# Optimization experiments

Measured on AMD Instinct MI355X. Metric: run time of the kernel, lower is better.

The kernel has to match this reference:

```python
import jax, jax.numpy as jnp
import numpy as np

B, T, E, H = 4, 4096, 1024, 16
D = E // H          # per-head hidden_size in fla LinearAttention (num_heads=1)
CH = 64             # fused-chunk chunk size


def setup_inputs() -> dict:
    key = jax.random.key(0)
    k1, k2, k3, k4, k5 = jax.random.split(key, 5)
    s = 1.0 / np.sqrt(D).astype(np.float32)
    x = jax.random.normal(k1, (B, T, E), dtype=jnp.float32)
    Wq = jax.random.normal(k2, (D, D), dtype=jnp.float32) * s
    Wk = jax.random.normal(k3, (D, D), dtype=jnp.float32) * s
    Wv = jax.random.normal(k4, (D, D), dtype=jnp.float32) * s
    Wo = jax.random.normal(k5, (D, D), dtype=jnp.float32) * s
    return {"x": x, "Wq": Wq, "Wk": Wk, "Wv": Wv, "Wo": Wo}


def _phi(x):
    # fla 'elu' feature map: elu(x) + 1 (positive features)
    return jax.nn.elu(x) + 1.0


def _linear_attn_fused_chunk(q, k, v):
    # q,k,v: [B,H,T,D]; causal linear attention via chunked recurrence.
    b, h, t, d = q.shape
    n = t // CH
    # [N, B, H, CH, D] so scan runs over chunks
    qc = q.reshape(b, h, n, CH, d).transpose(2, 0, 1, 3, 4)
    kc = k.reshape(b, h, n, CH, d).transpose(2, 0, 1, 3, 4)
    vc = v.reshape(b, h, n, CH, d).transpose(2, 0, 1, 3, 4)
    mask = jnp.tril(jnp.ones((CH, CH), dtype=q.dtype))  # causal, diag inclusive

    def step(S, inp):
        qi, ki, vi = inp                                   # [B,H,CH,D]
        attn = jnp.einsum('bhck,bhek->bhce', qi, ki) * mask  # intra-chunk scores
        o_intra = jnp.einsum('bhce,bhed->bhcd', attn, vi)
        o_inter = jnp.einsum('bhck,bhkd->bhcd', qi, S)       # past-state term
        S_new = S + jnp.einsum('bhck,bhcd->bhkd', ki, vi)    # state update
        return S_new, o_intra + o_inter

    S0 = jnp.zeros((b, h, d, d), dtype=q.dtype)
    _, oc = jax.lax.scan(step, S0, (qc, kc, vc))           # oc: [N,B,H,CH,D]
    return oc.transpose(1, 2, 0, 3, 4).reshape(b, h, t, d)


def reference(x, Wq, Wk, Wv, Wo):
    # split outer heads: [B,T,E] -> [B,H,T,D]
    xh = x.reshape(B, T, H, D).transpose(0, 2, 1, 3)
    # shared [D,D] projections (fla LinearAttention with num_heads=1), tied elu feature map on q,k
    q = _phi(jnp.einsum('bhtd,de->bhte', xh, Wq))
    k = _phi(jnp.einsum('bhtd,de->bhte', xh, Wk))
    v = jnp.einsum('bhtd,de->bhte', xh, Wv)
    o = _linear_attn_fused_chunk(q, k, v)                  # no feature-map norm, identity output norm
    o = jnp.einsum('bhtd,de->bhte', o, Wo)
    return o.transpose(0, 2, 1, 3).reshape(B, T, E)
```

## Files before the change

kernel.cpp:

```cpp
#include <hip/hip_runtime.h>
#include <cstdint>
#include <cstddef>

constexpr int Bc = 4, Tc = 4096, Ec = 1024, Hc = 16, Dc = 64, CHc = 64;
constexpr int NSEG = 16;
constexpr int SEGT = Tc / NSEG;
constexpr int NCHUNK = SEGT / CHc;
constexpr int LP = 72;

typedef __attribute__((ext_vector_type(8))) short short8;
typedef __attribute__((ext_vector_type(4))) short short4v;
typedef __attribute__((ext_vector_type(4))) float f32x4;

__device__ __forceinline__ unsigned short f2bf(float f) {
  union { float f; unsigned int u; } v; v.f = f;
  return (unsigned short)((v.u + 0x7FFFu + ((v.u >> 16) & 1u)) >> 16);
}
__device__ __forceinline__ float bf2f(unsigned short u) {
  union { unsigned int u; float f; } v; v.u = ((unsigned int)u) << 16;
  return v.f;
}
__device__ __forceinline__ float phi_elu1(float x) {
  return x > 0.f ? x + 1.f : __expf(x);
}
__device__ __forceinline__ short8 ld8(const unsigned short* p) {
  return *reinterpret_cast<const short8*>(p);
}
__device__ __forceinline__ void st8(unsigned short* p, short8 v) {
  *reinterpret_cast<short8*>(p) = v;
}

#define MFMA_B16(a, b, c) __builtin_amdgcn_mfma_f32_16x16x32_bf16((a), (b), (c), 0, 0, 0)

__device__ __forceinline__ void cvt_store16(unsigned short* dst, float4 f0, float4 f1,
                                            float4 f2, float4 f3) {
  union { unsigned short us[16]; short8 v[2]; } pk;
  pk.us[0] = f2bf(f0.x);  pk.us[1] = f2bf(f0.y);  pk.us[2] = f2bf(f0.z);  pk.us[3] = f2bf(f0.w);
  pk.us[4] = f2bf(f1.x);  pk.us[5] = f2bf(f1.y);  pk.us[6] = f2bf(f1.z);  pk.us[7] = f2bf(f1.w);
  pk.us[8] = f2bf(f2.x);  pk.us[9] = f2bf(f2.y);  pk.us[10] = f2bf(f2.z); pk.us[11] = f2bf(f2.w);
  pk.us[12] = f2bf(f3.x); pk.us[13] = f2bf(f3.y); pk.us[14] = f2bf(f3.z); pk.us[15] = f2bf(f3.w);
  st8(dst, pk.v[0]); st8(dst + 8, pk.v[1]);
}

__global__ void prep_weights(const float* __restrict__ Wq, const float* __restrict__ Wk,
                             const float* __restrict__ Wv, const float* __restrict__ Wo,
                             unsigned short* __restrict__ wT) {
  int tid = blockIdx.x * blockDim.x + threadIdx.x;
  if (tid >= 4 * Dc * Dc) return;
  int m = tid >> 12, i = tid & 4095, d = i >> 6, e = i & 63;
  const float* W = (m == 0) ? Wq : (m == 1) ? Wk : (m == 2) ? Wv : Wo;
  wT[m * 4096 + e * 64 + d] = f2bf(W[d * 64 + e]);
}

__global__ __launch_bounds__(256, 3) void pass1_kvseg(
    const float* __restrict__ x, const unsigned short* __restrict__ wT,
    float* __restrict__ kvseg) {
  __shared__ unsigned short s_x[2 * 64 * LP];
  __shared__ unsigned short s_kT[64 * LP];
  __shared__ unsigned short s_vT[64 * LP];

  const int tid = threadIdx.x;
  const int w = tid >> 6, lane = tid & 63, lr = lane & 15, lq = lane >> 4;
  const int bh = blockIdx.x, sg = blockIdx.y;
  const int b = bh >> 4, h = bh & 15;
  const float* xbase = x + ((size_t)b * Tc + (size_t)sg * SEGT) * Ec + h * Dc;
  const unsigned short* wkT = wT + 4096;
  const unsigned short* wvT = wT + 2 * 4096;
  const int sr = tid >> 2, sc = tid & 3;
  const f32x4 zero4 = {0.f, 0.f, 0.f, 0.f};

  short8 awk[2], awv[2];
#pragma unroll
  for (int kk = 0; kk < 2; ++kk) {
    awk[kk] = ld8(wkT + (w * 16 + lr) * 64 + kk * 32 + lq * 8);
    awv[kk] = ld8(wvT + (w * 16 + lr) * 64 + kk * 32 + lq * 8);
  }

  {
    const float4* xf = reinterpret_cast<const float4*>(xbase + (size_t)sr * Ec + sc * 16);
    cvt_store16(&s_x[sr * LP + sc * 16], xf[0], xf[1], xf[2], xf[3]);
  }
  __syncthreads();

  f32x4 sacc[4] = {zero4, zero4, zero4, zero4};

#pragma unroll
  for (int ci = 0; ci < NCHUNK; ++ci) {
    unsigned short* sxc = &s_x[(ci & 1) * 64 * LP];
    unsigned short* sxn = &s_x[(1 - (ci & 1)) * 64 * LP];

    float4 pf0, pf1, pf2, pf3;
    if (ci < NCHUNK - 1) {
      const float4* xf = reinterpret_cast<const float4*>(
          xbase + (size_t)((ci + 1) * CHc + sr) * Ec + sc * 16);
      pf0 = xf[0]; pf1 = xf[1]; pf2 = xf[2]; pf3 = xf[3];
    }

    f32x4 ak[4] = {zero4, zero4, zero4, zero4};
    f32x4 av[4] = {zero4, zero4, zero4, zero4};
#pragma unroll
    for (int c = 0; c < 4; ++c) {
#pragma unroll
      for (int kk = 0; kk < 2; ++kk) {
        short8 bx = ld8(&sxc[(c * 16 + lr) * LP + kk * 32 + lq * 8]);
        ak[c] = MFMA_B16(awk[kk], bx, ak[c]);
        av[c] = MFMA_B16(awv[kk], bx, av[c]);
      }
    }
#pragma unroll
    for (int c = 0; c < 4; ++c) {
#pragma unroll
      for (int j = 0; j < 4; ++j) {
        int r = w * 16 + lq * 4 + j;
        s_kT[r * LP + c * 16 + lr] = f2bf(phi_elu1(ak[c][j]));
        s_vT[r * LP + c * 16 + lr] = f2bf(av[c][j]);
      }
    }
    __syncthreads();

    short8 avt[2];
#pragma unroll
    for (int kk = 0; kk < 2; ++kk)
      avt[kk] = ld8(&s_vT[(w * 16 + lr) * LP + kk * 32 + lq * 8]);
#pragma unroll
    for (int c = 0; c < 4; ++c)
#pragma unroll
      for (int kk = 0; kk < 2; ++kk)
        sacc[c] = MFMA_B16(avt[kk], ld8(&s_kT[(c * 16 + lr) * LP + kk * 32 + lq * 8]), sacc[c]);

    if (ci < NCHUNK - 1)
      cvt_store16(&sxn[sr * LP + sc * 16], pf0, pf1, pf2, pf3);
    __syncthreads();
  }

  float* dst = kvseg + ((size_t)(bh * NSEG + sg)) * 4096;
#pragma unroll
  for (int c = 0; c < 4; ++c)
#pragma unroll
    for (int j = 0; j < 4; ++j)
      dst[(w * 16 + lq * 4 + j) * 64 + c * 16 + lr] = sacc[c][j];
}

__global__ __launch_bounds__(256) void pass2_prefix(const float* __restrict__ kvseg,
                                                    unsigned short* __restrict__ sprefix) {
  const int bh = blockIdx.x, tile = blockIdx.y;
  const int e = tile * 1024 + threadIdx.x * 4;
  const float* src = kvseg + (size_t)bh * NSEG * 4096 + e;
  unsigned short* dst = sprefix + (size_t)bh * NSEG * 4096 + e;
  float4 vals[NSEG];
#pragma unroll
  for (int s = 0; s < NSEG; ++s)
    vals[s] = *reinterpret_cast<const float4*>(src + (size_t)s * 4096);
  float a0 = 0.f, a1 = 0.f, a2 = 0.f, a3 = 0.f;
#pragma unroll
  for (int s = 0; s < NSEG; ++s) {
    short4v sv;
    sv[0] = (short)f2bf(a0); sv[1] = (short)f2bf(a1);
    sv[2] = (short)f2bf(a2); sv[3] = (short)f2bf(a3);
    *reinterpret_cast<short4v*>(dst + (size_t)s * 4096) = sv;
    a0 += vals[s].x; a1 += vals[s].y; a2 += vals[s].z; a3 += vals[s].w;
  }
}

__global__ __launch_bounds__(256, 2) void pass3_main(
    const float* __restrict__ x, const unsigned short* __restrict__ wT,
    const unsigned short* __restrict__ sprefix, float* __restrict__ out) {
  __shared__ unsigned short s_x[2 * 64 * LP];
  __shared__ unsigned short s_q [64 * LP];
  __shared__ unsigned short s_k [64 * LP];
  __shared__ unsigned short s_kT[64 * LP];
  __shared__ unsigned short s_vT[64 * LP];
  __shared__ unsigned short s_Sb[64 * LP];

  const int tid = threadIdx.x;
  const int w = tid >> 6, lane = tid & 63, lr = lane & 15, lq = lane >> 4;
  const int bh = blockIdx.x, sg = blockIdx.y;
  const int b = bh >> 4, h = bh & 15;
  const float* xbase = x + ((size_t)b * Tc + (size_t)sg * SEGT) * Ec + h * Dc;
  float* obase = out + ((size_t)b * Tc + (size_t)sg * SEGT) * Ec + h * Dc;
  const unsigned short* wqT = wT;
  const unsigned short* wkT = wT + 4096;
  const unsigned short* wvT = wT + 2 * 4096;
  const unsigned short* woT = wT + 3 * 4096;
  const unsigned short* Sg = sprefix + ((size_t)(bh * NSEG + sg)) * 4096;
  const int sr = tid >> 2, sc = tid & 3;
  const int arow = (w * 16 + lr) * LP;
  const f32x4 zero4 = {0.f, 0.f, 0.f, 0.f};

  short8 bwq[4][2], bwk[4][2], bwo[4][2], awv[2];
#pragma unroll
  for (int c = 0; c < 4; ++c) {
#pragma unroll
    for (int kk = 0; kk < 2; ++kk) {
      bwq[c][kk] = ld8(wqT + (c * 16 + lr) * 64 + kk * 32 + lq * 8);
      bwk[c][kk] = ld8(wkT + (c * 16 + lr) * 64 + kk * 32 + lq * 8);
      bwo[c][kk] = ld8(woT + (c * 16 + lr) * 64 + kk * 32 + lq * 8);
    }
  }
#pragma unroll
  for (int kk = 0; kk < 2; ++kk)
    awv[kk] = ld8(wvT + (w * 16 + lr) * 64 + kk * 32 + lq * 8);

  {
    const float4* xf = reinterpret_cast<const float4*>(xbase + (size_t)sr * Ec + sc * 16);
    cvt_store16(&s_x[sr * LP + sc * 16], xf[0], xf[1], xf[2], xf[3]);
    const unsigned short* sp = Sg + sr * 64 + (tid & 3) * 16;
    st8(&s_Sb[sr * LP + (tid & 3) * 16], ld8(sp));
    st8(&s_Sb[sr * LP + (tid & 3) * 16 + 8], ld8(sp + 8));
  }
  __syncthreads();

  f32x4 sacc[4];
#pragma unroll
  for (int c = 0; c < 4; ++c)
#pragma unroll
    for (int j = 0; j < 4; ++j)
      sacc[c][j] = bf2f(s_Sb[(w * 16 + lq * 4 + j) * LP + c * 16 + lr]);

#pragma unroll
  for (int ci = 0; ci < NCHUNK; ++ci) {
    unsigned short* sxc = &s_x[(ci & 1) * 64 * LP];
    unsigned short* sxn = &s_x[(1 - (ci & 1)) * 64 * LP];

    float4 pf0, pf1, pf2, pf3;
    if (ci < NCHUNK - 1) {
      const float4* xf = reinterpret_cast<const float4*>(
          xbase + (size_t)((ci + 1) * CHc + sr) * Ec + sc * 16);
      pf0 = xf[0]; pf1 = xf[1]; pf2 = xf[2]; pf3 = xf[3];
    }

    short8 ax[2];
    ax[0] = ld8(&sxc[arow + 0 + lq * 8]);
    ax[1] = ld8(&sxc[arow + 32 + lq * 8]);
    f32x4 aq[4]  = {zero4, zero4, zero4, zero4};
    f32x4 ack[4] = {zero4, zero4, zero4, zero4};
    f32x4 acv[4] = {zero4, zero4, zero4, zero4};
#pragma unroll
    for (int c = 0; c < 4; ++c) {
#pragma unroll
      for (int kk = 0; kk < 2; ++kk) {
        aq[c]  = MFMA_B16(ax[kk],  bwq[c][kk], aq[c]);
        ack[c] = MFMA_B16(ax[kk],  bwk[c][kk], ack[c]);
        acv[c] = MFMA_B16(awv[kk], ld8(&sxc[(c * 16 + lr) * LP + kk * 32 + lq * 8]), acv[c]);
      }
    }
#pragma unroll
    for (int c = 0; c < 4; ++c) {
#pragma unroll
      for (int j = 0; j < 4; ++j) {
        int r = w * 16 + lq * 4 + j;
        float kv2 = phi_elu1(ack[c][j]);
        s_q [r * LP + c * 16 + lr] = f2bf(phi_elu1(aq[c][j]));
        s_k [r * LP + c * 16 + lr] = f2bf(kv2);
        s_kT[(c * 16 + lr) * LP + r] = f2bf(kv2);
        s_vT[r * LP + c * 16 + lr] = f2bf(acv[c][j]);
      }
    }
    __syncthreads();

    short8 a_q[2], a_v[2];
#pragma unroll
    for (int kk = 0; kk < 2; ++kk) {
      a_q[kk] = ld8(&s_q[arow + kk * 32 + lq * 8]);
      a_v[kk] = ld8(&s_vT[arow + kk * 32 + lq * 8]);
    }
    f32x4 aat[4] = {zero4, zero4, zero4, zero4};
    f32x4 ao[4]  = {zero4, zero4, zero4, zero4};
#pragma unroll
    for (int c = 0; c < 4; ++c) {
      const int br = (c * 16 + lr) * LP;
#pragma unroll
      for (int kk = 0; kk < 2; ++kk) {
        aat[c]  = MFMA_B16(a_q[kk], ld8(&s_k[br + kk * 32 + lq * 8]), aat[c]);
        ao[c]   = MFMA_B16(a_q[kk], ld8(&s_Sb[br + kk * 32 + lq * 8]), ao[c]);
        sacc[c] = MFMA_B16(a_v[kk], ld8(&s_kT[br + kk * 32 + lq * 8]), sacc[c]);
      }
    }
#pragma unroll
    for (int c = 0; c < 4; ++c) {
#pragma unroll
      for (int j = 0; j < 4; ++j) {
        int t = w * 16 + lq * 4 + j, tp = c * 16 + lr;
        sxc[t * LP + tp] = f2bf((tp <= t) ? aat[c][j] : 0.f);
      }
    }
    __syncthreads();

    short8 a_at[2];
#pragma unroll
    for (int kk = 0; kk < 2; ++kk)
      a_at[kk] = ld8(&sxc[arow + kk * 32 + lq * 8]);
#pragma unroll
    for (int c = 0; c < 4; ++c)
#pragma unroll
      for (int kk = 0; kk < 2; ++kk)
        ao[c] = MFMA_B16(a_at[kk], ld8(&s_vT[(c * 16 + lr) * LP + kk * 32 + lq * 8]), ao[c]);
#pragma unroll
    for (int c = 0; c < 4; ++c) {
#pragma unroll
      for (int j = 0; j < 4; ++j) {
        int r = w * 16 + lq * 4 + j;
        s_q[r * LP + c * 16 + lr] = f2bf(ao[c][j]);
        if (ci < NCHUNK - 1)
          s_Sb[r * LP + c * 16 + lr] = f2bf(sacc[c][j]);
      }
    }
    __syncthreads();

    short8 a_o[2];
#pragma unroll
    for (int kk = 0; kk < 2; ++kk)
      a_o[kk] = ld8(&s_q[arow + kk * 32 + lq * 8]);
    f32x4 aou[4] = {zero4, zero4, zero4, zero4};
#pragma unroll
    for (int c = 0; c < 4; ++c)
#pragma unroll
      for (int kk = 0; kk < 2; ++kk)
        aou[c] = MFMA_B16(a_o[kk], bwo[c][kk], aou[c]);
    float* orow = obase + (size_t)(ci * CHc) * Ec;
#pragma unroll
    for (int c = 0; c < 4; ++c)
#pragma unroll
      for (int j = 0; j < 4; ++j)
        orow[(size_t)(w * 16 + lq * 4 + j) * Ec + c * 16 + lr] = aou[c][j];

    if (ci < NCHUNK - 1)
      cvt_store16(&sxn[sr * LP + sc * 16], pf0, pf1, pf2, pf3);
    __syncthreads();
  }
}

extern "C" void kernel_launch(void* const* d_in, const int* in_sizes, int n_in,
                              void* d_out, int out_size, void* d_ws, size_t ws_size,
                              hipStream_t stream) {
  const float* x  = (const float*)d_in[0];
  const float* Wq = (const float*)d_in[1];
  const float* Wk = (const float*)d_in[2];
  const float* Wv = (const float*)d_in[3];
  const float* Wo = (const float*)d_in[4];
  float* out = (float*)d_out;

  unsigned short* wT = (unsigned short*)d_ws;
  float* kvseg = (float*)((char*)d_ws + 32768);
  unsigned short* sprefix = (unsigned short*)((char*)d_ws + 32768 + (size_t)16 * 1024 * 1024);

  prep_weights<<<dim3(64), dim3(256), 0, stream>>>(Wq, Wk, Wv, Wo, wT);
  pass1_kvseg<<<dim3(64, NSEG), dim3(256), 0, stream>>>(x, wT, kvseg);
  pass2_prefix<<<dim3(64, 4), dim3(256), 0, stream>>>(kvseg, sprefix);
  pass3_main<<<dim3(64, NSEG), dim3(256), 0, stream>>>(x, wT, sprefix, out);
}
```

Baseline: 74.09 us.

## Fold Wo into Wv, load x directly into registers, pack bf16 stores

Precomputes Wv·Wo as a single weight so the output projection GEMM and one barrier stage disappear from the main loop. This is valid because the attention output is linear in v. Pass1 now loads x straight from global into MFMA operand registers instead of staging it through shared memory. Layouts are transposed so shared-memory writes become packed 4-wide bf16 stores rather than scalar ones. The cost is a fused weight rounded to bf16 and a different numerical path.

```diff
diff --git a/kernel.cpp b/kernel.cpp
--- a/kernel.cpp
+++ b/kernel.cpp
@@ -9,13 +9,15 @@
 constexpr int LP = 72;
 
 typedef __attribute__((ext_vector_type(8))) short short8;
-typedef __attribute__((ext_vector_type(4))) short short4v;
 typedef __attribute__((ext_vector_type(4))) float f32x4;
 
 __device__ __forceinline__ unsigned short f2bf(float f) {
   union { float f; unsigned int u; } v; v.f = f;
   return (unsigned short)((v.u + 0x7FFFu + ((v.u >> 16) & 1u)) >> 16);
 }
+__device__ __forceinline__ unsigned int pk2(float lo, float hi) {
+  return ((unsigned int)f2bf(hi) << 16) | (unsigned int)f2bf(lo);
+}
 __device__ __forceinline__ float bf2f(unsigned short u) {
   union { unsigned int u; float f; } v; v.u = ((unsigned int)u) << 16;
   return v.f;
@@ -26,113 +28,92 @@
 __device__ __forceinline__ short8 ld8(const unsigned short* p) {
   return *reinterpret_cast<const short8*>(p);
 }
-__device__ __forceinline__ void st8(unsigned short* p, short8 v) {
-  *reinterpret_cast<short8*>(p) = v;
-}
-
-#define MFMA_B16(a, b, c) __builtin_amdgcn_mfma_f32_16x16x32_bf16((a), (b), (c), 0, 0, 0)
-
-__device__ __forceinline__ void cvt_store16(unsigned short* dst, float4 f0, float4 f1,
-                                            float4 f2, float4 f3) {
-  union { unsigned short us[16]; short8 v[2]; } pk;
-  pk.us[0] = f2bf(f0.x);  pk.us[1] = f2bf(f0.y);  pk.us[2] = f2bf(f0.z);  pk.us[3] = f2bf(f0.w);
-  pk.us[4] = f2bf(f1.x);  pk.us[5] = f2bf(f1.y);  pk.us[6] = f2bf(f1.z);  pk.us[7] = f2bf(f1.w);
-  pk.us[8] = f2bf(f2.x);  pk.us[9] = f2bf(f2.y);  pk.us[10] = f2bf(f2.z); pk.us[11] = f2bf(f2.w);
-  pk.us[12] = f2bf(f3.x); pk.us[13] = f2bf(f3.y); pk.us[14] = f2bf(f3.z); pk.us[15] = f2bf(f3.w);
-  st8(dst, pk.v[0]); st8(dst + 8, pk.v[1]);
-}
+__device__ __forceinline__ short8 pk8(float4 a, float4 b) {
+  union { unsigned int u[4]; short8 s; } r;
+  r.u[0] = pk2(a.x, a.y); r.u[1] = pk2(a.z, a.w);
+  r.u[2] = pk2(b.x, b.y); r.u[3] = pk2(b.z, b.w);
+  return r.s;
+}
+__device__ __forceinline__ void st4(unsigned short* p, float v0, float v1, float v2, float v3) {
+  union { unsigned int u[2]; uint2 t; } r;
+  r.u[0] = pk2(v0, v1); r.u[1] = pk2(v2, v3);
+  *reinterpret_cast<uint2*>(p) = r.t;
+}
+
+#define MFMA(a, b, c) __builtin_amdgcn_mfma_f32_16x16x32_bf16((a), (b), (c), 0, 0, 0)
 
 __global__ void prep_weights(const float* __restrict__ Wq, const float* __restrict__ Wk,
                              const float* __restrict__ Wv, const float* __restrict__ Wo,
-                             unsigned short* __restrict__ wT) {
-  int tid = blockIdx.x * blockDim.x + threadIdx.x;
-  if (tid >= 4 * Dc * Dc) return;
-  int m = tid >> 12, i = tid & 4095, d = i >> 6, e = i & 63;
-  const float* W = (m == 0) ? Wq : (m == 1) ? Wk : (m == 2) ? Wv : Wo;
-  wT[m * 4096 + e * 64 + d] = f2bf(W[d * 64 + e]);
+                             unsigned short* __restrict__ wbuf) {
+  int gid = blockIdx.x * 256 + threadIdx.x;
+  int m = gid >> 12, i = gid & 4095, r = i >> 6, c = i & 63;
+  if (m == 0) {
+    wbuf[i] = f2bf(Wq[c * 64 + r]);
+  } else if (m == 1) {
+    wbuf[4096 + i] = f2bf(Wk[c * 64 + r]);
+  } else {
+    float acc = 0.f;
+    for (int g = 0; g < 64; ++g) acc += Wv[c * 64 + g] * Wo[g * 64 + r];
+    wbuf[8192 + i] = f2bf(acc);
+  }
 }
 
 __global__ __launch_bounds__(256, 3) void pass1_kvseg(
-    const float* __restrict__ x, const unsigned short* __restrict__ wT,
+    const float* __restrict__ x, const unsigned short* __restrict__ wbuf,
     float* __restrict__ kvseg) {
-  __shared__ unsigned short s_x[2 * 64 * LP];
   __shared__ unsigned short s_kT[64 * LP];
   __shared__ unsigned short s_vT[64 * LP];
-
-  const int tid = threadIdx.x;
-  const int w = tid >> 6, lane = tid & 63, lr = lane & 15, lq = lane >> 4;
-  const int bh = blockIdx.x, sg = blockIdx.y;
-  const int b = bh >> 4, h = bh & 15;
+  const int tid = threadIdx.x, w = tid >> 6, lane = tid & 63, lr = lane & 15, lq = lane >> 4;
+  const int bh = blockIdx.x, sg = blockIdx.y, b = bh >> 4, h = bh & 15;
   const float* xbase = x + ((size_t)b * Tc + (size_t)sg * SEGT) * Ec + h * Dc;
-  const unsigned short* wkT = wT + 4096;
-  const unsigned short* wvT = wT + 2 * 4096;
-  const int sr = tid >> 2, sc = tid & 3;
-  const f32x4 zero4 = {0.f, 0.f, 0.f, 0.f};
-
-  short8 awk[2], awv[2];
-#pragma unroll
-  for (int kk = 0; kk < 2; ++kk) {
-    awk[kk] = ld8(wkT + (w * 16 + lr) * 64 + kk * 32 + lq * 8);
-    awv[kk] = ld8(wvT + (w * 16 + lr) * 64 + kk * 32 + lq * 8);
-  }
-
-  {
-    const float4* xf = reinterpret_cast<const float4*>(xbase + (size_t)sr * Ec + sc * 16);
-    cvt_store16(&s_x[sr * LP + sc * 16], xf[0], xf[1], xf[2], xf[3]);
-  }
-  __syncthreads();
-
-  f32x4 sacc[4] = {zero4, zero4, zero4, zero4};
-
+  const unsigned short* wkT = wbuf + 4096;
+  const unsigned short* wvoT = wbuf + 8192;
+  const f32x4 Z = {0.f, 0.f, 0.f, 0.f};
+
+  short8 bwk[4][2], bwv[4][2];
+#pragma unroll
+  for (int c = 0; c < 4; ++c)
+#pragma unroll
+    for (int kk = 0; kk < 2; ++kk) {
+      bwk[c][kk] = ld8(wkT + (c * 16 + lr) * 64 + kk * 32 + lq * 8);
+      bwv[c][kk] = ld8(wvoT + (c * 16 + lr) * 64 + kk * 32 + lq * 8);
+    }
+
+  const float* xr = xbase + (size_t)(w * 16 + lr) * Ec + lq * 8;
+  float4 p0 = ((const float4*)xr)[0], p1 = ((const float4*)xr)[1];
+  float4 p2 = ((const float4*)(xr + 32))[0], p3 = ((const float4*)(xr + 32))[1];
+
+  f32x4 sacc[4] = {Z, Z, Z, Z};
 #pragma unroll
   for (int ci = 0; ci < NCHUNK; ++ci) {
-    unsigned short* sxc = &s_x[(ci & 1) * 64 * LP];
-    unsigned short* sxn = &s_x[(1 - (ci & 1)) * 64 * LP];
-
-    float4 pf0, pf1, pf2, pf3;
+    short8 xa0 = pk8(p0, p1), xa1 = pk8(p2, p3);
     if (ci < NCHUNK - 1) {
-      const float4* xf = reinterpret_cast<const float4*>(
-          xbase + (size_t)((ci + 1) * CHc + sr) * Ec + sc * 16);
-      pf0 = xf[0]; pf1 = xf[1]; pf2 = xf[2]; pf3 = xf[3];
-    }
-
-    f32x4 ak[4] = {zero4, zero4, zero4, zero4};
-    f32x4 av[4] = {zero4, zero4, zero4, zero4};
-#pragma unroll
-    for (int c = 0; c < 4; ++c) {
-#pragma unroll
-      for (int kk = 0; kk < 2; ++kk) {
-        short8 bx = ld8(&sxc[(c * 16 + lr) * LP + kk * 32 + lq * 8]);
-        ak[c] = MFMA_B16(awk[kk], bx, ak[c]);
-        av[c] = MFMA_B16(awv[kk], bx, av[c]);
-      }
-    }
-#pragma unroll
-    for (int c = 0; c < 4; ++c) {
-#pragma unroll
-      for (int j = 0; j < 4; ++j) {
-        int r = w * 16 + lq * 4 + j;
-        s_kT[r * LP + c * 16 + lr] = f2bf(phi_elu1(ak[c][j]));
-        s_vT[r * LP + c * 16 + lr] = f2bf(av[c][j]);
-      }
-    }
-    __syncthreads();
-
-    short8 avt[2];
-#pragma unroll
-    for (int kk = 0; kk < 2; ++kk)
-      avt[kk] = ld8(&s_vT[(w * 16 + lr) * LP + kk * 32 + lq * 8]);
-#pragma unroll
-    for (int c = 0; c < 4; ++c)
-#pragma unroll
-      for (int kk = 0; kk < 2; ++kk)
-        sacc[c] = MFMA_B16(avt[kk], ld8(&s_kT[(c * 16 + lr) * LP + kk * 32 + lq * 8]), sacc[c]);
-
-    if (ci < NCHUNK - 1)
-      cvt_store16(&sxn[sr * LP + sc * 16], pf0, pf1, pf2, pf3);
-    __syncthreads();
-  }
-
+      const float* nr = xbase + (size_t)((ci + 1) * CHc + w * 16 + lr) * Ec + lq * 8;
+      p0 = ((const float4*)nr)[0]; p1 = ((const float4*)nr)[1];
+      p2 = ((const float4*)(nr + 32))[0]; p3 = ((const float4*)(nr + 32))[1];
+    }
+    f32x4 ak[4] = {Z, Z, Z, Z}, av[4] = {Z, Z, Z, Z};
+#pragma unroll
+    for (int c = 0; c < 4; ++c) {
+      ak[c] = MFMA(xa0, bwk[c][0], ak[c]); ak[c] = MFMA(xa1, bwk[c][1], ak[c]);
+      av[c] = MFMA(xa0, bwv[c][0], av[c]); av[c] = MFMA(xa1, bwv[c][1], av[c]);
+    }
+#pragma unroll
+    for (int c = 0; c < 4; ++c) {
+      int o = (c * 16 + lr) * LP + w * 16 + lq * 4;
+      st4(&s_kT[o], phi_elu1(ak[c][0]), phi_elu1(ak[c][1]), phi_elu1(ak[c][2]), phi_elu1(ak[c][3]));
+      st4(&s_vT[o], av[c][0], av[c][1], av[c][2], av[c][3]);
+    }
+    __syncthreads();
+    short8 akt0 = ld8(&s_kT[(w * 16 + lr) * LP + lq * 8]);
+    short8 akt1 = ld8(&s_kT[(w * 16 + lr) * LP + 32 + lq * 8]);
+#pragma unroll
+    for (int c = 0; c < 4; ++c) {
+      sacc[c] = MFMA(akt0, ld8(&s_vT[(c * 16 + lr) * LP + lq * 8]), sacc[c]);
+      sacc[c] = MFMA(akt1, ld8(&s_vT[(c * 16 + lr) * LP + 32 + lq * 8]), sacc[c]);
+    }
+    __syncthreads();
+  }
   float* dst = kvseg + ((size_t)(bh * NSEG + sg)) * 4096;
 #pragma unroll
   for (int c = 0; c < 4; ++c)
@@ -149,183 +130,152 @@
   unsigned short* dst = sprefix + (size_t)bh * NSEG * 4096 + e;
   float4 vals[NSEG];
 #pragma unroll
-  for (int s = 0; s < NSEG; ++s)
-    vals[s] = *reinterpret_cast<const float4*>(src + (size_t)s * 4096);
+  for (int s = 0; s < NSEG; ++s) vals[s] = *(const float4*)(src + (size_t)s * 4096);
   float a0 = 0.f, a1 = 0.f, a2 = 0.f, a3 = 0.f;
 #pragma unroll
   for (int s = 0; s < NSEG; ++s) {
-    short4v sv;
-    sv[0] = (short)f2bf(a0); sv[1] = (short)f2bf(a1);
-    sv[2] = (short)f2bf(a2); sv[3] = (short)f2bf(a3);
-    *reinterpret_cast<short4v*>(dst + (size_t)s * 4096) = sv;
+    union { unsigned int u[2]; uint2 t; } r;
+    r.u[0] = pk2(a0, a1); r.u[1] = pk2(a2, a3);
+    *reinterpret_cast<uint2*>(dst + (size_t)s * 4096) = r.t;
     a0 += vals[s].x; a1 += vals[s].y; a2 += vals[s].z; a3 += vals[s].w;
   }
 }
 
 __global__ __launch_bounds__(256, 2) void pass3_main(
-    const float* __restrict__ x, const unsigned short* __restrict__ wT,
+    const float* __restrict__ x, const unsigned short* __restrict__ wbuf,
     const unsigned short* __restrict__ sprefix, float* __restrict__ out) {
-  __shared__ unsigned short s_x[2 * 64 * LP];
+  __shared__ unsigned short s_x [64 * LP];
   __shared__ unsigned short s_q [64 * LP];
   __shared__ unsigned short s_k [64 * LP];
   __shared__ unsigned short s_kT[64 * LP];
   __shared__ unsigned short s_vT[64 * LP];
   __shared__ unsigned short s_Sb[64 * LP];
-
-  const int tid = threadIdx.x;
-  const int w = tid >> 6, lane = tid & 63, lr = lane & 15, lq = lane >> 4;
-  const int bh = blockIdx.x, sg = blockIdx.y;
-  const int b = bh >> 4, h = bh & 15;
+  __shared__ unsigned short s_at[64 * LP];
+
+  const int tid = threadIdx.x, w = tid >> 6, lane = tid & 63, lr = lane & 15, lq = lane >> 4;
+  const int bh = blockIdx.x, sg = blockIdx.y, b = bh >> 4, h = bh & 15;
   const float* xbase = x + ((size_t)b * Tc + (size_t)sg * SEGT) * Ec + h * Dc;
   float* obase = out + ((size_t)b * Tc + (size_t)sg * SEGT) * Ec + h * Dc;
-  const unsigned short* wqT = wT;
-  const unsigned short* wkT = wT + 4096;
-  const unsigned short* wvT = wT + 2 * 4096;
-  const unsigned short* woT = wT + 3 * 4096;
+  const unsigned short* wqT = wbuf;
+  const unsigned short* wkT = wbuf + 4096;
+  const unsigned short* wvoT = wbuf + 8192;
   const unsigned short* Sg = sprefix + ((size_t)(bh * NSEG + sg)) * 4096;
   const int sr = tid >> 2, sc = tid & 3;
-  const int arow = (w * 16 + lr) * LP;
-  const f32x4 zero4 = {0.f, 0.f, 0.f, 0.f};
-
-  short8 bwq[4][2], bwk[4][2], bwo[4][2], awv[2];
-#pragma unroll
-  for (int c = 0; c < 4; ++c) {
+  const f32x4 Z = {0.f, 0.f, 0.f, 0.f};
+
+  f32x4 sacc[4];
+#pragma unroll
+  for (int c = 0; c < 4; ++c)
+#pragma unroll
+    for (int j = 0; j < 4; ++j)
+      sacc[c][j] = bf2f(Sg[(w * 16 + lq * 4 + j) * 64 + c * 16 + lr]);
+
+  short8 awq[2], awk[2], bwk[4][2], bwv[4][2];
+#pragma unroll
+  for (int kk = 0; kk < 2; ++kk) {
+    awq[kk] = ld8(wqT + (w * 16 + lr) * 64 + kk * 32 + lq * 8);
+    awk[kk] = ld8(wkT + (w * 16 + lr) * 64 + kk * 32 + lq * 8);
+  }
+#pragma unroll
+  for (int c = 0; c < 4; ++c)
 #pragma unroll
     for (int kk = 0; kk < 2; ++kk) {
-      bwq[c][kk] = ld8(wqT + (c * 16 + lr) * 64 + kk * 32 + lq * 8);
       bwk[c][kk] = ld8(wkT + (c * 16 + lr) * 64 + kk * 32 + lq * 8);
-      bwo[c][kk] = ld8(woT + (c * 16 + lr) * 64 + kk * 32 + lq * 8);
-    }
-  }
-#pragma unroll
-  for (int kk = 0; kk < 2; ++kk)
-    awv[kk] = ld8(wvT + (w * 16 + lr) * 64 + kk * 32 + lq * 8);
+      bwv[c][kk] = ld8(wvoT + (c * 16 + lr) * 64 + kk * 32 + lq * 8);
+    }
 
   {
-    const float4* xf = reinterpret_cast<const float4*>(xbase + (size_t)sr * Ec + sc * 16);
-    cvt_store16(&s_x[sr * LP + sc * 16], xf[0], xf[1], xf[2], xf[3]);
-    const unsigned short* sp = Sg + sr * 64 + (tid & 3) * 16;
-    st8(&s_Sb[sr * LP + (tid & 3) * 16], ld8(sp));
-    st8(&s_Sb[sr * LP + (tid & 3) * 16 + 8], ld8(sp + 8));
+    const float4* xf = (const float4*)(xbase + (size_t)sr * Ec + sc * 16);
+    float4 f0 = xf[0], f1 = xf[1], f2 = xf[2], f3 = xf[3];
+    *(short8*)&s_x[sr * LP + sc * 16] = pk8(f0, f1);
+    *(short8*)&s_x[sr * LP + sc * 16 + 8] = pk8(f2, f3);
   }
   __syncthreads();
 
-  f32x4 sacc[4];
-#pragma unroll
-  for (int c = 0; c < 4; ++c)
-#pragma unroll
-    for (int j = 0; j < 4; ++j)
-      sacc[c][j] = bf2f(s_Sb[(w * 16 + lq * 4 + j) * LP + c * 16 + lr]);
-
 #pragma unroll
   for (int ci = 0; ci < NCHUNK; ++ci) {
-    unsigned short* sxc = &s_x[(ci & 1) * 64 * LP];
-    unsigned short* sxn = &s_x[(1 - (ci & 1)) * 64 * LP];
-
     float4 pf0, pf1, pf2, pf3;
     if (ci < NCHUNK - 1) {
-      const float4* xf = reinterpret_cast<const float4*>(
-          xbase + (size_t)((ci + 1) * CHc + sr) * Ec + sc * 16);
+      const float4* xf = (const float4*)(xbase + (size_t)((ci + 1) * CHc + sr) * Ec + sc * 16);
       pf0 = xf[0]; pf1 = xf[1]; pf2 = xf[2]; pf3 = xf[3];
     }
 
-    short8 ax[2];
-    ax[0] = ld8(&sxc[arow + 0 + lq * 8]);
-    ax[1] = ld8(&sxc[arow + 32 + lq * 8]);
-    f32x4 aq[4]  = {zero4, zero4, zero4, zero4};
-    f32x4 ack[4] = {zero4, zero4, zero4, zero4};
-    f32x4 acv[4] = {zero4, zero4, zero4, zero4};
-#pragma unroll
-    for (int c = 0; c < 4; ++c) {
-#pragma unroll
-      for (int kk = 0; kk < 2; ++kk) {
-        aq[c]  = MFMA_B16(ax[kk],  bwq[c][kk], aq[c]);
-        ack[c] = MFMA_B16(ax[kk],  bwk[c][kk], ack[c]);
-        acv[c] = MFMA_B16(awv[kk], ld8(&sxc[(c * 16 + lr) * LP + kk * 32 + lq * 8]), acv[c]);
-      }
-    }
-#pragma unroll
-    for (int c = 0; c < 4; ++c) {
-#pragma unroll
-      for (int j = 0; j < 4; ++j) {
-        int r = w * 16 + lq * 4 + j;
-        float kv2 = phi_elu1(ack[c][j]);
-        s_q [r * LP + c * 16 + lr] = f2bf(phi_elu1(aq[c][j]));
-        s_k [r * LP + c * 16 + lr] = f2bf(kv2);
-        s_kT[(c * 16 + lr) * LP + r] = f2bf(kv2);
-        s_vT[r * LP + c * 16 + lr] = f2bf(acv[c][j]);
-      }
-    }
-    __syncthreads();
-
-    short8 a_q[2], a_v[2];
-#pragma unroll
-    for (int kk = 0; kk < 2; ++kk) {
-      a_q[kk] = ld8(&s_q[arow + kk * 32 + lq * 8]);
-      a_v[kk] = ld8(&s_vT[arow + kk * 32 + lq * 8]);
-    }
-    f32x4 aat[4] = {zero4, zero4, zero4, zero4};
-    f32x4 ao[4]  = {zero4, zero4, zero4, zero4};
+    short8 xb[4][2];
+#pragma unroll
+    for (int c = 0; c < 4; ++c) {
+      xb[c][0] = ld8(&s_x[(c * 16 + lr) * LP + lq * 8]);
+      xb[c][1] = ld8(&s_x[(c * 16 + lr) * LP + 32 + lq * 8]);
+    }
+    short8 xw0 = ld8(&s_x[(w * 16 + lr) * LP + lq * 8]);
+    short8 xw1 = ld8(&s_x[(w * 16 + lr) * LP + 32 + lq * 8]);
+#pragma unroll
+    for (int c = 0; c < 4; ++c)
+      st4(&s_Sb[(c * 16 + lr) * LP + w * 16 + lq * 4], sacc[c][0], sacc[c][1], sacc[c][2], sacc[c][3]);
+
+    f32x4 aqt[4] = {Z, Z, Z, Z}, akt[4] = {Z, Z, Z, Z}, ack[4] = {Z, Z, Z, Z}, acv[4] = {Z, Z, Z, Z};
+#pragma unroll
+    for (int c = 0; c < 4; ++c) {
+      aqt[c] = MFMA(awq[0], xb[c][0], aqt[c]); aqt[c] = MFMA(awq[1], xb[c][1], aqt[c]);
+      akt[c] = MFMA(awk[0], xb[c][0], akt[c]); akt[c] = MFMA(awk[1], xb[c][1], akt[c]);
+      ack[c] = MFMA(xw0, bwk[c][0], ack[c]);   ack[c] = MFMA(xw1, bwk[c][1], ack[c]);
+      acv[c] = MFMA(xw0, bwv[c][0], acv[c]);   acv[c] = MFMA(xw1, bwv[c][1], acv[c]);
+    }
+#pragma unroll
+    for (int c = 0; c < 4; ++c) {
+      int o = (c * 16 + lr) * LP + w * 16 + lq * 4;
+      st4(&s_q [o], phi_elu1(aqt[c][0]), phi_elu1(aqt[c][1]), phi_elu1(aqt[c][2]), phi_elu1(aqt[c][3]));
+      st4(&s_k [o], phi_elu1(akt[c][0]), phi_elu1(akt[c][1]), phi_elu1(akt[c][2]), phi_elu1(akt[c][3]));
+      st4(&s_kT[o], phi_elu1(ack[c][0]), phi_elu1(ack[c][1]), phi_elu1(ack[c][2]), phi_elu1(ack[c][3]));
+      st4(&s_vT[o], acv[c][0], acv[c][1], acv[c][2], acv[c][3]);
+    }
+    __syncthreads();
+
+    short8 a_q0 = ld8(&s_q [(w * 16 + lr) * LP + lq * 8]);
+    short8 a_q1 = ld8(&s_q [(w * 16 + lr) * LP + 32 + lq * 8]);
+    short8 a_k0 = ld8(&s_k [(w * 16 + lr) * LP + lq * 8]);
+    short8 a_k1 = ld8(&s_k [(w * 16 + lr) * LP + 32 + lq * 8]);
+    short8 a_t0 = ld8(&s_kT[(w * 16 + lr) * LP + lq * 8]);
+    short8 a_t1 = ld8(&s_kT[(w * 16 + lr) * LP + 32 + lq * 8]);
+    f32x4 aat[4] = {Z, Z, Z, Z}, ao[4] = {Z, Z, Z, Z};
 #pragma unroll
     for (int c = 0; c < 4; ++c) {
       const int br = (c * 16 + lr) * LP;
-#pragma unroll
-      for (int kk = 0; kk < 2; ++kk) {
-        aat[c]  = MFMA_B16(a_q[kk], ld8(&s_k[br + kk * 32 + lq * 8]), aat[c]);
-        ao[c]   = MFMA_B16(a_q[kk], ld8(&s_Sb[br + kk * 32 + lq * 8]), ao[c]);
-        sacc[c] = MFMA_B16(a_v[kk], ld8(&s_kT[br + kk * 32 + lq * 8]), sacc[c]);
-      }
-    }
-#pragma unroll
-    for (int c = 0; c < 4; ++c) {
-#pragma unroll
-      for (int j = 0; j < 4; ++j) {
-        int t = w * 16 + lq * 4 + j, tp = c * 16 + lr;
-        sxc[t * LP + tp] = f2bf((tp <= t) ? aat[c][j] : 0.f);
-      }
-    }
-    __syncthreads();
-
-    short8 a_at[2];
-#pragma unroll
-    for (int kk = 0; kk < 2; ++kk)
-      a_at[kk] = ld8(&sxc[arow + kk * 32 + lq * 8]);
+      aat[c]  = MFMA(a_k0, ld8(&s_q [br + lq * 8]), aat[c]);
+      aat[c]  = MFMA(a_k1, ld8(&s_q [br + 32 + lq * 8]), aat[c]);
+      ao[c]   = MFMA(a_q0, ld8(&s_Sb[br + lq * 8]), ao[c]);
+      ao[c]   = MFMA(a_q1, ld8(&s_Sb[br + 32 + lq * 8]), ao[c]);
+      sacc[c] = MFMA(a_t0, ld8(&s_vT[br + lq * 8]), sacc[c]);
+      sacc[c] = MFMA(a_t1, ld8(&s_vT[br + 32 + lq * 8]), sacc[c]);
+    }
+#pragma unroll
+    for (int c = 0; c < 4; ++c) {
+      int t = c * 16 + lr, tp = w * 16 + lq * 4;
+      float m0 = (tp + 0 <= t) ? aat[c][0] : 0.f;
+      float m1 = (tp + 1 <= t) ? aat[c][1] : 0.f;
+      float m2 = (tp + 2 <= t) ? aat[c][2] : 0.f;
+      float m3 = (tp + 3 <= t) ? aat[c][3] : 0.f;
+      st4(&s_at[t * LP + tp], m0, m1, m2, m3);
+    }
+    __syncthreads();
+
+    short8 a_a0 = ld8(&s_at[(w * 16 + lr) * LP + lq * 8]);
+    short8 a_a1 = ld8(&s_at[(w * 16 + lr) * LP + 32 + lq * 8]);
+#pragma unroll
+    for (int c = 0; c < 4; ++c) {
+      const int br = (c * 16 + lr) * LP;
+      ao[c] = MFMA(a_a0, ld8(&s_vT[br + lq * 8]), ao[c]);
+      ao[c] = MFMA(a_a1, ld8(&s_vT[br + 32 + lq * 8]), ao[c]);
+    }
+    float* orow = obase + (size_t)(ci * CHc) * Ec;
 #pragma unroll
     for (int c = 0; c < 4; ++c)
 #pragma unroll
-      for (int kk = 0; kk < 2; ++kk)
-        ao[c] = MFMA_B16(a_at[kk], ld8(&s_vT[(c * 16 + lr) * LP + kk * 32 + lq * 8]), ao[c]);
-#pragma unroll
-    for (int c = 0; c < 4; ++c) {
-#pragma unroll
-      for (int j = 0; j < 4; ++j) {
-        int r = w * 16 + lq * 4 + j;
-        s_q[r * LP + c * 16 + lr] = f2bf(ao[c][j]);
-        if (ci < NCHUNK - 1)
-          s_Sb[r * LP + c * 16 + lr] = f2bf(sacc[c][j]);
-      }
-    }
-    __syncthreads();
-
-    short8 a_o[2];
-#pragma unroll
-    for (int kk = 0; kk < 2; ++kk)
-      a_o[kk] = ld8(&s_q[arow + kk * 32 + lq * 8]);
-    f32x4 aou[4] = {zero4, zero4, zero4, zero4};
-#pragma unroll
-    for (int c = 0; c < 4; ++c)
-#pragma unroll
-      for (int kk = 0; kk < 2; ++kk)
-        aou[c] = MFMA_B16(a_o[kk], bwo[c][kk], aou[c]);
-    float* orow = obase + (size_t)(ci * CHc) * Ec;
-#pragma unroll
-    for (int c = 0; c < 4; ++c)
-#pragma unroll
       for (int j = 0; j < 4; ++j)
-        orow[(size_t)(w * 16 + lq * 4 + j) * Ec + c * 16 + lr] = aou[c][j];
-
-    if (ci < NCHUNK - 1)
-      cvt_store16(&sxn[sr * LP + sc * 16], pf0, pf1, pf2, pf3);
+        orow[(size_t)(w * 16 + lq * 4 + j) * Ec + c * 16 + lr] = ao[c][j];
+    if (ci < NCHUNK - 1) {
+      *(short8*)&s_x[sr * LP + sc * 16] = pk8(pf0, pf1);
+      *(short8*)&s_x[sr * LP + sc * 16 + 8] = pk8(pf2, pf3);
+    }
     __syncthreads();
   }
 }
@@ -340,12 +290,12 @@
   const float* Wo = (const float*)d_in[4];
   float* out = (float*)d_out;
 
-  unsigned short* wT = (unsigned short*)d_ws;
+  unsigned short* wbuf = (unsigned short*)d_ws;
   float* kvseg = (float*)((char*)d_ws + 32768);
   unsigned short* sprefix = (unsigned short*)((char*)d_ws + 32768 + (size_t)16 * 1024 * 1024);
 
-  prep_weights<<<dim3(64), dim3(256), 0, stream>>>(Wq, Wk, Wv, Wo, wT);
-  pass1_kvseg<<<dim3(64, NSEG), dim3(256), 0, stream>>>(x, wT, kvseg);
+  prep_weights<<<dim3(48), dim3(256), 0, stream>>>(Wq, Wk, Wv, Wo, wbuf);
+  pass1_kvseg<<<dim3(64, NSEG), dim3(256), 0, stream>>>(x, wbuf, kvseg);
   pass2_prefix<<<dim3(64, 4), dim3(256), 0, stream>>>(kvseg, sprefix);
-  pass3_main<<<dim3(64, NSEG), dim3(256), 0, stream>>>(x, wT, sprefix, out);
-}
+  pass3_main<<<dim3(64, NSEG), dim3(256), 0, stream>>>(x, wbuf, sprefix, out);
+}
```

After: 79.52 us. 1.07x slower.
